# Performance work log

Measured on AMD Instinct MI355X. Metric: run time of the kernel, lower is better.

## Reference

```python
import jax, jax.numpy as jnp
import numpy as np


def setup_inputs() -> dict:
    key = jax.random.key(0)
    k1, k2, k3, k4 = jax.random.split(key, 4)
    B, I, P, F = 4096, 1024, 512, 2048
    x = jax.random.normal(k1, (B, I), dtype=jnp.float32)
    # params initialized like torch.rand(...)*2-1 (uniform in [-1,1])
    features = jax.random.uniform(k2, (F, I), dtype=jnp.float32, minval=-1.0, maxval=1.0)
    prototypes = jax.random.uniform(k3, (P, I), dtype=jnp.float32, minval=-1.0, maxval=1.0)
    # scalars: torch inits to zeros; use small nonzero values so output/grads are informative
    abt = jax.random.normal(k4, (3,), dtype=jnp.float32) * 0.1
    alpha = abt[0:1]
    beta = abt[1:2]
    theta = abt[2:3]
    return {"x": x, "features": features, "prototypes": prototypes,
            "alpha": alpha, "beta": beta, "theta": theta}


def reference(x, features, prototypes, alpha, beta, theta):
    # x: [b, i], features: [f, i], prototypes: [p, i]
    # Original einsums broadcast over p but the projection is p-independent:
    xf = x @ features.T            # [b, f]
    pf = prototypes @ features.T   # [p, f]
    x_pres = jax.nn.relu(xf)       # [b, f]
    p_pres = jax.nn.relu(pf)       # [p, f]
    # common[b,p]       = sum_f xf*pf*relu(xf)*relu(pf)
    # x_distinct[b,p]   = sum_f xf*relu(xf)*(1-relu(pf))
    # p_distinct[b,p]   = sum_f pf*relu(pf)*(1-relu(xf))
    a = xf * x_pres                # [b, f]
    c = pf * p_pres                # [p, f]
    common = a @ c.T                                   # [b, p]
    x_distinctive = a @ (1.0 - p_pres).T               # [b, p]
    p_distinctive = (1.0 - x_pres) @ c.T               # [b, p]
    return theta * common - alpha * x_distinctive - beta * p_distinctive
```

## Files before the change

kernel.cpp:

```cpp
#include <hip/hip_runtime.h>
#include <cstdint>

typedef __attribute__((ext_vector_type(8))) short bf16x8;
typedef __attribute__((ext_vector_type(16))) float f32x16;
typedef __attribute__((ext_vector_type(4))) float f4;
typedef __attribute__((ext_vector_type(8))) unsigned short u16x8;
typedef unsigned short u16;


__device__ __forceinline__ u16 f2bf(float f) {
  uint32_t u = __builtin_bit_cast(uint32_t, f);
  u += 0x7fffu + ((u >> 16) & 1u);
  return (u16)(u >> 16);
}

__device__ __forceinline__ float bf2f(u16 h) {
  return __builtin_bit_cast(float, (uint32_t)h << 16);
}

__device__ __forceinline__ void async_cp16(const void* g, void* l) {
  __builtin_amdgcn_global_load_lds(
      (const __attribute__((address_space(1))) uint32_t*)g,
      (__attribute__((address_space(3))) uint32_t*)l, 16, 0, 0);
}

__global__ __launch_bounds__(256) void cast3(
    const float* __restrict__ x, const float* __restrict__ f,
    const float* __restrict__ p, u16* __restrict__ dst,
    int n1, int n2, int n3) {
  int i = (blockIdx.x * 256 + threadIdx.x) * 8;
  const float* src;
  int local;
  if (i < n1) { src = x; local = i; }
  else if (i < n1 + n2) { src = f; local = i - n1; }
  else if (i < n1 + n2 + n3) { src = p; local = i - n1 - n2; }
  else return;
  f4 a = *(const f4*)(src + local);
  f4 b = *(const f4*)(src + local + 4);
  u16x8 o;
  o[0] = f2bf(a.x); o[1] = f2bf(a.y); o[2] = f2bf(a.z); o[3] = f2bf(a.w);
  o[4] = f2bf(b.x); o[5] = f2bf(b.y); o[6] = f2bf(b.z); o[7] = f2bf(b.w);
  *(u16x8*)(dst + i) = o;
}


__device__ __forceinline__ void stage_tile(
    const u16* __restrict__ A, const u16* __restrict__ B, int K,
    int k0, int tid, u16* L) {
  constexpr int TM = 128, TN = 128;
  const int wave = tid >> 6;
  #pragma unroll
  for (int it = 0; it < TM / 32; ++it) {
    int c = it * 256 + tid;
    int row = c >> 3, pc = c & 7;
    int gc = pc ^ (row & 7);
    async_cp16(A + (size_t)row * K + (k0 + gc * 8),
               &L[(it * 256 + wave * 64) * 8]);
  }
  #pragma unroll
  for (int it = 0; it < TN / 32; ++it) {
    int c = it * 256 + tid;
    int row = c >> 3, pc = c & 7;
    int gc = pc ^ (row & 7);
    async_cp16(B + (size_t)row * K + (k0 + gc * 8),
               &L[TM * 64 + (it * 256 + wave * 64) * 8]);
  }
}

__device__ __forceinline__ void compute_tile(
    const u16* L, int lane, int wrow, int wcol, f32x16 (&acc)[2][2]) {
  constexpr int TM = 128;
  #pragma unroll
  for (int s = 0; s < 4; ++s) {
    const int h = s * 2 + (lane >> 5);
    bf16x8 bfr[2], afr[2];
    #pragma unroll
    for (int j = 0; j < 2; ++j) {
      const int rb = wcol * 64 + j * 32 + (lane & 31);
      bfr[j] = *(const bf16x8*)&L[TM * 64 + (rb * 8 + (h ^ (rb & 7))) * 8];
    }
    #pragma unroll
    for (int i = 0; i < 2; ++i) {
      const int ra = wrow * 64 + i * 32 + (lane & 31);
      afr[i] = *(const bf16x8*)&L[(ra * 8 + (h ^ (ra & 7))) * 8];
    }
    #pragma unroll
    for (int i = 0; i < 2; ++i)
      #pragma unroll
      for (int j = 0; j < 2; ++j)
        acc[i][j] = __builtin_amdgcn_mfma_f32_32x32x16_bf16(
            afr[i], bfr[j], acc[i][j], 0, 0, 0);
  }
}

__device__ __forceinline__ void mainloop(
    const u16* __restrict__ A, const u16* __restrict__ B, int K,
    int kbeg, int kend, int tid, u16* lds, f32x16 (&acc)[2][2]) {
  constexpr int BK = 64;
  constexpr int BUF = 16384;
  const int lane = tid & 63;
  const int wave = tid >> 6;
  const int wrow = wave >> 1, wcol = wave & 1;

  stage_tile(A, B, K, kbeg, tid, lds);
  int cur = 0;
  for (int k0 = kbeg; k0 < kend; k0 += BK) {
    if (k0 + BK < kend) {
      stage_tile(A, B, K, k0 + BK, tid, lds + (cur ^ 1) * BUF);
      asm volatile("s_waitcnt vmcnt(8)" ::: "memory");
    } else {
      asm volatile("s_waitcnt vmcnt(0)" ::: "memory");
    }
    __builtin_amdgcn_s_barrier();
    compute_tile(lds + cur * BUF, lane, wrow, wcol, acc);
    __builtin_amdgcn_s_barrier();
    cur ^= 1;
  }
}


__device__ __forceinline__ void stage_unit32(
    const u16* __restrict__ M, int K, int k0, int tid, u16* Lbase) {
  #pragma unroll
  for (int it = 0; it < 2; ++it) {
    int c = it * 512 + tid;
    int row = c >> 2, pc = c & 3;
    int gc = pc ^ ((row >> 1) & 3);
    async_cp16(M + (size_t)row * K + (k0 + gc * 8),
               &Lbase[(it * 512 + (tid >> 6) * 64) * 8]);
  }
}

__device__ __forceinline__ void mainloop32(
    const u16* __restrict__ A, const u16* __restrict__ B, int K,
    int kbeg, int tid, u16* lds, f32x16 (&acc)[4][2]) {
  constexpr int NT = 16;
  constexpr int BUFS = 16384;
  const int lane = tid & 63;
  const int wave = tid >> 6;
  const int wrow = wave >> 2, wcol = wave & 3;

  #pragma unroll
  for (int p = 0; p < 3; ++p) {
    stage_unit32(A, K, kbeg + p * 32, tid, lds + p * BUFS);
    stage_unit32(B, K, kbeg + p * 32, tid, lds + p * BUFS + 8192);
  }
  asm volatile("s_waitcnt vmcnt(8)" ::: "memory");
  __builtin_amdgcn_s_barrier();

  for (int t = 0; t < NT; ++t) {
    const u16* L = lds + (t & 3) * BUFS;
    u16* Lnxt = lds + ((t + 3) & 3) * BUFS;
    const int k3 = kbeg + (t + 3) * 32;
    #pragma unroll
    for (int s = 0; s < 2; ++s) {
      const int h = s * 2 + (lane >> 5);
      bf16x8 bfr[2], afr[4];
      #pragma unroll
      for (int j = 0; j < 2; ++j) {
        const int rb = wcol * 64 + j * 32 + (lane & 31);
        bfr[j] = *(const bf16x8*)&L[8192 + (rb * 4 + (h ^ ((rb >> 1) & 3))) * 8];
      }
      #pragma unroll
      for (int i = 0; i < 4; ++i) {
        const int ra = wrow * 128 + i * 32 + (lane & 31);
        afr[i] = *(const bf16x8*)&L[(ra * 4 + (h ^ ((ra >> 1) & 3))) * 8];
      }
      if (t < NT - 3) {
        if (s == 0) stage_unit32(A, K, k3, tid, Lnxt);
        else        stage_unit32(B, K, k3, tid, Lnxt + 8192);
      }
      __builtin_amdgcn_s_barrier();
      asm volatile("s_waitcnt lgkmcnt(0)" ::: "memory");
      __builtin_amdgcn_sched_barrier(0);
      __builtin_amdgcn_s_setprio(1);
      #pragma unroll
      for (int i = 0; i < 4; ++i)
        #pragma unroll
        for (int j = 0; j < 2; ++j)
          acc[i][j] = __builtin_amdgcn_mfma_f32_32x32x16_bf16(
              afr[i], bfr[j], acc[i][j], 0, 0, 0);
      __builtin_amdgcn_s_setprio(0);
      if (s == 1) {
        if (t < NT - 3)       asm volatile("s_waitcnt vmcnt(8)" ::: "memory");
        else if (t == NT - 3) asm volatile("s_waitcnt vmcnt(4)" ::: "memory");
        else if (t == NT - 2) asm volatile("s_waitcnt vmcnt(0)" ::: "memory");
      }
      __builtin_amdgcn_s_barrier();
    }
  }
}


__global__ __launch_bounds__(256) void gemm12(
    const u16* __restrict__ xb, const u16* __restrict__ pb,
    const u16* __restrict__ fb, u16* __restrict__ Acat, u16* __restrict__ Bcat,
    const float* __restrict__ alpha, const float* __restrict__ beta,
    const float* __restrict__ theta) {
  constexpr int TM = 128, K = 1024, N = 2048;
  constexpr int TSTRIDE = 136;
  __shared__ u16 lds[32768];

  const int tid = threadIdx.x;
  const int lane = tid & 63;
  const int wave = tid >> 6;
  const int wrow = wave >> 1, wcol = wave & 1;

  const int bid = blockIdx.x;
  const int xcd = bid & 7, slot = bid >> 3;
  const int xt = (xcd & 3) * 9 + (slot >> 3);
  const int yt = (xcd >> 2) * 8 + (slot & 7);

  const int bm_all = xt * TM;
  const int bn = yt * 128;
  const bool is_x = bm_all < 4096;
  const u16* A = is_x ? xb + (size_t)bm_all * K : pb + (size_t)(bm_all - 4096) * K;
  const u16* B = fb + (size_t)bn * K;

  f32x16 acc[2][2] = {};
  mainloop(A, B, K, 0, K, tid, lds, acc);

  float th = 0.f, al = 0.f, be = 0.f;
  if (!is_x) { th = theta[0]; al = alpha[0]; be = beta[0]; }
  u16* dst = is_x ? Acat : Bcat;
  const int rowbase = is_x ? bm_all : bm_all - 4096;
  const int rquad = 4 * (lane >> 5);

  #pragma unroll
  for (int half = 0; half < 2; ++half) {
    __syncthreads();
    #pragma unroll
    for (int i = 0; i < 2; ++i) {
      #pragma unroll
      for (int j = 0; j < 2; ++j) {
        const int cl = wcol * 64 + j * 32 + (lane & 31);
        #pragma unroll
        for (int r = 0; r < 16; ++r) {
          const int rl = wrow * 64 + i * 32 + (r & 3) + 8 * (r >> 2) + rquad;
          float v = acc[i][j][r];
          float pres = v > 0.f ? v : 0.f;
          float o;
          if (is_x) o = half == 0 ? v * pres : 1.f - pres;
          else {
            float cc = v * pres;
            o = half == 0 ? th * cc - al * (1.f - pres) : -be * cc;
          }
          lds[rl * TSTRIDE + cl] = f2bf(o);
        }
      }
    }
    __syncthreads();
    #pragma unroll
    for (int v = 0; v < 8; ++v) {
      const int rl = v * 16 + (tid >> 4);
      const int c8 = (tid & 15) * 8;
      u16x8 vec = *(const u16x8*)&lds[rl * TSTRIDE + c8];
      *(u16x8*)&dst[(size_t)(rowbase + rl) * (2 * N) + bn + c8 + half * N] = vec;
    }
  }
}

__global__ __launch_bounds__(512) void gemm3(
    const u16* __restrict__ Acat, const u16* __restrict__ Bcat,
    u16* __restrict__ part) {
  constexpr int K = 4096, KSPLIT = 8;
  __shared__ u16 lds[65536];

  const int tid = threadIdx.x;
  const int bid = blockIdx.x;
  const int bz = bid & 7;
  const int slot = bid >> 3;
  const int bxt = slot & 15;
  const int byt = slot >> 4;

  const int bm = bxt * 256;
  const int bn = byt * 256;
  const int kbeg = bz * (K / KSPLIT);

  f32x16 acc[4][2] = {};
  mainloop32(Acat + (size_t)bm * K, Bcat + (size_t)bn * K, K, kbeg,
             tid, lds, acc);

  const int tileId = byt * 16 + bxt;
  const size_t pbase = ((size_t)bz * 32 + tileId) * 65536;
  #pragma unroll
  for (int i = 0; i < 4; ++i)
    #pragma unroll
    for (int j = 0; j < 2; ++j)
      #pragma unroll
      for (int h = 0; h < 2; ++h) {
        u16x8 o;
        #pragma unroll
        for (int e = 0; e < 8; ++e) o[e] = f2bf(acc[i][j][h * 8 + e]);
        *(u16x8*)&part[pbase + (size_t)(i * 4 + j * 2 + h) * 4096 + tid * 8] = o;
      }
}

__global__ __launch_bounds__(512) void reduce4(
    const u16* __restrict__ part, float* __restrict__ out) {
  constexpr int N = 512;
  const int tid = threadIdx.x;
  const int lane = tid & 63;
  const int wave = tid >> 6;
  const int wrow = wave >> 2, wcol = wave & 3;
  const int tileId = blockIdx.x >> 4;
  const int q = blockIdx.x & 15;
  const int bm = (tileId & 15) * 256;
  const int bn = (tileId >> 4) * 256;

  float v[8] = {};
  #pragma unroll
  for (int z = 0; z < 8; ++z) {
    u16x8 u = *(const u16x8*)&part[((size_t)z * 32 + tileId) * 65536 +
                                   (size_t)q * 4096 + tid * 8];
    #pragma unroll
    for (int e = 0; e < 8; ++e) v[e] += bf2f(u[e]);
  }
  const int i = q >> 2, j = (q >> 1) & 1, h = q & 1;
  const int gc = bn + wcol * 64 + j * 32 + (lane & 31);
  const int grb = bm + wrow * 128 + i * 32 + 4 * (lane >> 5);
  #pragma unroll
  for (int e = 0; e < 8; ++e) {
    const int reg = h * 8 + e;
    out[(size_t)(grb + (reg & 3) + 8 * (reg >> 2)) * N + gc] = v[e];
  }
}

extern "C" void kernel_launch(void* const* d_in, const int* in_sizes, int n_in,
                              void* d_out, int out_size, void* d_ws, size_t ws_size,
                              hipStream_t stream) {
  const float* x     = (const float*)d_in[0];
  const float* feat  = (const float*)d_in[1];
  const float* proto = (const float*)d_in[2];
  const float* alpha = (const float*)d_in[3];
  const float* beta  = (const float*)d_in[4];
  const float* theta = (const float*)d_in[5];
  float* out = (float*)d_out;

  constexpr int Bb = 4096, Ii = 1024, Pp = 512, Ff = 2048;

  char* ws = (char*)d_ws;
  u16* xb   = (u16*)ws;
  u16* fb   = xb + (size_t)Bb * Ii;
  u16* pb   = fb + (size_t)Ff * Ii;
  size_t r0 = 33554432;
  u16* Acat = (u16*)(ws + r0);
  u16* Bcat = Acat + (size_t)Bb * 2 * Ff;
  u16* part = Bcat + (size_t)Pp * 2 * Ff;

  const int n1 = Bb * Ii, n2 = Ff * Ii, n3 = Pp * Ii;
  cast3<<<((n1 + n2 + n3) / 8 + 255) / 256, 256, 0, stream>>>(
      x, feat, proto, xb, n1, n2, n3);

  gemm12<<<576, 256, 0, stream>>>(xb, pb, fb, Acat, Bcat, alpha, beta, theta);

  gemm3<<<256, 512, 0, stream>>>(Acat, Bcat, part);

  reduce4<<<512, 512, 0, stream>>>(part, out);
}
```

Before: 142.5 us.

## Replace double-buffered 128x128 GEMM mainloop with 4-slot BK=32 ring pipeline

Swaps the first GEMM's double-buffered BK=64 mainloop for a four-slot ring of BK=32 stages, prefetched three tiles ahead. Each stage's loads are split between the two MFMA sub-steps and protected by s_setprio and scheduled waitcnts, following the second GEMM's existing ring scheme. The goal is to hide global-load latency better and spread async copies across compute. In exchange, the loop runs twice as many iterations with more barriers, and the vmcnt bookkeeping is fragile.

```diff
diff --git a/kernel.cpp b/kernel.cpp
--- a/kernel.cpp
+++ b/kernel.cpp
@@ -44,81 +44,6 @@
 }
 
 
-__device__ __forceinline__ void stage_tile(
-    const u16* __restrict__ A, const u16* __restrict__ B, int K,
-    int k0, int tid, u16* L) {
-  constexpr int TM = 128, TN = 128;
-  const int wave = tid >> 6;
-  #pragma unroll
-  for (int it = 0; it < TM / 32; ++it) {
-    int c = it * 256 + tid;
-    int row = c >> 3, pc = c & 7;
-    int gc = pc ^ (row & 7);
-    async_cp16(A + (size_t)row * K + (k0 + gc * 8),
-               &L[(it * 256 + wave * 64) * 8]);
-  }
-  #pragma unroll
-  for (int it = 0; it < TN / 32; ++it) {
-    int c = it * 256 + tid;
-    int row = c >> 3, pc = c & 7;
-    int gc = pc ^ (row & 7);
-    async_cp16(B + (size_t)row * K + (k0 + gc * 8),
-               &L[TM * 64 + (it * 256 + wave * 64) * 8]);
-  }
-}
-
-__device__ __forceinline__ void compute_tile(
-    const u16* L, int lane, int wrow, int wcol, f32x16 (&acc)[2][2]) {
-  constexpr int TM = 128;
-  #pragma unroll
-  for (int s = 0; s < 4; ++s) {
-    const int h = s * 2 + (lane >> 5);
-    bf16x8 bfr[2], afr[2];
-    #pragma unroll
-    for (int j = 0; j < 2; ++j) {
-      const int rb = wcol * 64 + j * 32 + (lane & 31);
-      bfr[j] = *(const bf16x8*)&L[TM * 64 + (rb * 8 + (h ^ (rb & 7))) * 8];
-    }
-    #pragma unroll
-    for (int i = 0; i < 2; ++i) {
-      const int ra = wrow * 64 + i * 32 + (lane & 31);
-      afr[i] = *(const bf16x8*)&L[(ra * 8 + (h ^ (ra & 7))) * 8];
-    }
-    #pragma unroll
-    for (int i = 0; i < 2; ++i)
-      #pragma unroll
-      for (int j = 0; j < 2; ++j)
-        acc[i][j] = __builtin_amdgcn_mfma_f32_32x32x16_bf16(
-            afr[i], bfr[j], acc[i][j], 0, 0, 0);
-  }
-}
-
-__device__ __forceinline__ void mainloop(
-    const u16* __restrict__ A, const u16* __restrict__ B, int K,
-    int kbeg, int kend, int tid, u16* lds, f32x16 (&acc)[2][2]) {
-  constexpr int BK = 64;
-  constexpr int BUF = 16384;
-  const int lane = tid & 63;
-  const int wave = tid >> 6;
-  const int wrow = wave >> 1, wcol = wave & 1;
-
-  stage_tile(A, B, K, kbeg, tid, lds);
-  int cur = 0;
-  for (int k0 = kbeg; k0 < kend; k0 += BK) {
-    if (k0 + BK < kend) {
-      stage_tile(A, B, K, k0 + BK, tid, lds + (cur ^ 1) * BUF);
-      asm volatile("s_waitcnt vmcnt(8)" ::: "memory");
-    } else {
-      asm volatile("s_waitcnt vmcnt(0)" ::: "memory");
-    }
-    __builtin_amdgcn_s_barrier();
-    compute_tile(lds + cur * BUF, lane, wrow, wcol, acc);
-    __builtin_amdgcn_s_barrier();
-    cur ^= 1;
-  }
-}
-
-
 __device__ __forceinline__ void stage_unit32(
     const u16* __restrict__ M, int K, int k0, int tid, u16* Lbase) {
   #pragma unroll
@@ -128,6 +53,18 @@
     int gc = pc ^ ((row >> 1) & 3);
     async_cp16(M + (size_t)row * K + (k0 + gc * 8),
                &Lbase[(it * 512 + (tid >> 6) * 64) * 8]);
+  }
+}
+
+__device__ __forceinline__ void stage_unit128(
+    const u16* __restrict__ M, int K, int k0, int tid, u16* Lbase) {
+  #pragma unroll
+  for (int it = 0; it < 2; ++it) {
+    int c = it * 256 + tid;
+    int row = c >> 2, pc = c & 3;
+    int gc = pc ^ ((row >> 1) & 3);
+    async_cp16(M + (size_t)row * K + (k0 + gc * 8),
+               &Lbase[(it * 256 + (tid >> 6) * 64) * 8]);
   }
 }
 
@@ -191,6 +128,66 @@
   }
 }
 
+__device__ __forceinline__ void mainloop_ring128(
+    const u16* __restrict__ A, const u16* __restrict__ B, int K,
+    int tid, u16* lds, f32x16 (&acc)[2][2]) {
+  constexpr int NT = 32;
+  constexpr int BUFS = 8192;
+  const int lane = tid & 63;
+  const int wave = tid >> 6;
+  const int wrow = wave >> 1, wcol = wave & 1;
+
+  #pragma unroll
+  for (int p = 0; p < 3; ++p) {
+    stage_unit128(A, K, p * 32, tid, lds + p * BUFS);
+    stage_unit128(B, K, p * 32, tid, lds + p * BUFS + 4096);
+  }
+  asm volatile("s_waitcnt vmcnt(8)" ::: "memory");
+  __builtin_amdgcn_s_barrier();
+
+  for (int t = 0; t < NT; ++t) {
+    const u16* L = lds + (t & 3) * BUFS;
+    u16* Lnxt = lds + ((t + 3) & 3) * BUFS;
+    const int k3 = (t + 3) * 32;
+    #pragma unroll
+    for (int s = 0; s < 2; ++s) {
+      const int h = s * 2 + (lane >> 5);
+      bf16x8 bfr[2], afr[2];
+      #pragma unroll
+      for (int j = 0; j < 2; ++j) {
+        const int rb = wcol * 64 + j * 32 + (lane & 31);
+        bfr[j] = *(const bf16x8*)&L[4096 + (rb * 4 + (h ^ ((rb >> 1) & 3))) * 8];
+      }
+      #pragma unroll
+      for (int i = 0; i < 2; ++i) {
+        const int ra = wrow * 64 + i * 32 + (lane & 31);
+        afr[i] = *(const bf16x8*)&L[(ra * 4 + (h ^ ((ra >> 1) & 3))) * 8];
+      }
+      if (t < NT - 3) {
+        if (s == 0) stage_unit128(A, K, k3, tid, Lnxt);
+        else        stage_unit128(B, K, k3, tid, Lnxt + 4096);
+      }
+      __builtin_amdgcn_s_barrier();
+      asm volatile("s_waitcnt lgkmcnt(0)" ::: "memory");
+      __builtin_amdgcn_sched_barrier(0);
+      __builtin_amdgcn_s_setprio(1);
+      #pragma unroll
+      for (int i = 0; i < 2; ++i)
+        #pragma unroll
+        for (int j = 0; j < 2; ++j)
+          acc[i][j] = __builtin_amdgcn_mfma_f32_32x32x16_bf16(
+              afr[i], bfr[j], acc[i][j], 0, 0, 0);
+      __builtin_amdgcn_s_setprio(0);
+      if (s == 1) {
+        if (t < NT - 3)       asm volatile("s_waitcnt vmcnt(8)" ::: "memory");
+        else if (t == NT - 3) asm volatile("s_waitcnt vmcnt(4)" ::: "memory");
+        else if (t == NT - 2) asm volatile("s_waitcnt vmcnt(0)" ::: "memory");
+      }
+      __builtin_amdgcn_s_barrier();
+    }
+  }
+}
+
 
 __global__ __launch_bounds__(256) void gemm12(
     const u16* __restrict__ xb, const u16* __restrict__ pb,
@@ -218,7 +215,7 @@
   const u16* B = fb + (size_t)bn * K;
 
   f32x16 acc[2][2] = {};
-  mainloop(A, B, K, 0, K, tid, lds, acc);
+  mainloop_ring128(A, B, K, tid, lds, acc);
 
   float th = 0.f, al = 0.f, be = 0.f;
   if (!is_x) { th = theta[0]; al = alpha[0]; be = beta[0]; }
```

New measurement: 148.3 us. 1.04x slower.
